# Optimization experiments

Hardware: AMD Instinct MI355X
Metric: run time of the kernel (lower is better)

The kernel has to match this reference:

```python
import jax, jax.numpy as jnp
import numpy as np

N_SAMPLES = 8388608  # total packed samples across all rays
N_RAYS = 131072      # number of rays (segments)


def setup_inputs() -> dict:
    key = jax.random.key(0)
    k1, k2, k3 = jax.random.split(key, 3)
    # Sorted segment ids emulate the packed ray layout (samples of a ray are contiguous).
    segment_ids = jnp.sort(
        jax.random.randint(k1, (N_SAMPLES,), 0, N_RAYS, dtype=jnp.int32)
    )
    rgb_samples = jax.random.normal(k2, (N_SAMPLES, 3), dtype=jnp.float32)
    weights_samples = jax.random.uniform(k3, (N_SAMPLES, 1), dtype=jnp.float32)
    return {
        "segment_ids": segment_ids,
        "rgb_samples": rgb_samples,
        "weights_samples": weights_samples,
        "n_rays": N_RAYS,
    }


def reference(segment_ids, rgb_samples, weights_samples, n_rays):
    # pred_rgb[r] = sum over samples s belonging to ray r of w_s * rgb_s
    weighted = rgb_samples * weights_samples  # [N,3], weight broadcast over channels
    pred_rgb = jax.ops.segment_sum(weighted, segment_ids, num_segments=n_rays)  # [n_rays,3]
    return pred_rgb
```

## Files before the change

kernel.cpp:

```cpp
#include <hip/hip_runtime.h>


#define NTHREADS 256
#define SPT 16

__global__ __launch_bounds__(NTHREADS) void zero_out_kernel(float4* __restrict__ out4,
                                                            int n4) {
  int i = blockIdx.x * blockDim.x + threadIdx.x;
  if (i < n4) out4[i] = make_float4(0.f, 0.f, 0.f, 0.f);
}

__global__ __launch_bounds__(NTHREADS) void integrate_kernel(
    const int* __restrict__ ids, const float* __restrict__ rgb,
    const float* __restrict__ w, float* __restrict__ out, int n_samples) {
  const int lane = threadIdx.x & 63;
  const long long base = (long long)(blockIdx.x * blockDim.x + threadIdx.x) * SPT;

  int idv[SPT];
  float px[SPT], py[SPT], pz[SPT];

  if (base + (SPT - 1) < (long long)n_samples) {
    float ww[SPT], rr[3 * SPT];
    #pragma unroll
    for (int b = 0; b < SPT / 4; ++b) {
      const int4 t = *(const int4*)(ids + base + 4 * b);
      idv[4 * b + 0] = t.x; idv[4 * b + 1] = t.y;
      idv[4 * b + 2] = t.z; idv[4 * b + 3] = t.w;
    }
    #pragma unroll
    for (int b = 0; b < SPT / 4; ++b) {
      const float4 t = *(const float4*)(w + base + 4 * b);
      ww[4 * b + 0] = t.x; ww[4 * b + 1] = t.y;
      ww[4 * b + 2] = t.z; ww[4 * b + 3] = t.w;
    }
    #pragma unroll
    for (int m = 0; m < 3 * SPT / 4; ++m) {
      const float4 t = *(const float4*)(rgb + 3 * base + 4 * m);
      rr[4 * m + 0] = t.x; rr[4 * m + 1] = t.y;
      rr[4 * m + 2] = t.z; rr[4 * m + 3] = t.w;
    }
    #pragma unroll
    for (int k = 0; k < SPT; ++k) {
      px[k] = rr[3 * k + 0] * ww[k];
      py[k] = rr[3 * k + 1] * ww[k];
      pz[k] = rr[3 * k + 2] * ww[k];
    }
  } else {
    const int last = ids[n_samples - 1];
    #pragma unroll
    for (int j = 0; j < SPT; ++j) {
      const long long s = base + j;
      if (s < n_samples) {
        idv[j] = ids[s];
        const float t = w[s];
        px[j] = rgb[3 * s + 0] * t;
        py[j] = rgb[3 * s + 1] * t;
        pz[j] = rgb[3 * s + 2] * t;
      } else {
        idv[j] = (j == 0) ? last : idv[j - 1];
        px[j] = py[j] = pz[j] = 0.f;
      }
    }
  }

  const int first_id = idv[0];
  int run_id = first_id;
  float rx = px[0], ry = py[0], rz = pz[0];
  float hx = 0.f, hy = 0.f, hz = 0.f;
  bool f_intra = false;
  #pragma unroll
  for (int k = 1; k < SPT; ++k) {
    if (idv[k] == run_id) {
      rx += px[k]; ry += py[k]; rz += pz[k];
    } else {
      if (!f_intra) {
        hx = rx; hy = ry; hz = rz; f_intra = true;
      } else {
        atomicAdd(&out[3 * run_id + 0], rx);
        atomicAdd(&out[3 * run_id + 1], ry);
        atomicAdd(&out[3 * run_id + 2], rz);
      }
      run_id = idv[k];
      rx = px[k]; ry = py[k]; rz = pz[k];
    }
  }
  const int last_id = run_id;

  const int prev_tid = __shfl_up(last_id, 1, 64);
  int fl = (lane == 0 || f_intra || prev_tid != first_id) ? 1 : 0;
  float sx = rx, sy = ry, sz = rz;
  #pragma unroll
  for (int off = 1; off < 64; off <<= 1) {
    const float ox = __shfl_up(sx, off, 64);
    const float oy = __shfl_up(sy, off, 64);
    const float oz = __shfl_up(sz, off, 64);
    const int ofl = __shfl_up(fl, off, 64);
    if (lane >= off && fl == 0) { sx += ox; sy += oy; sz += oz; fl = ofl; }
  }

  const float pSx = __shfl_up(sx, 1, 64);
  const float pSy = __shfl_up(sy, 1, 64);
  const float pSz = __shfl_up(sz, 1, 64);
  if (f_intra) {
    const bool link = (lane > 0) && (prev_tid == first_id);
    atomicAdd(&out[3 * first_id + 0], hx + (link ? pSx : 0.f));
    atomicAdd(&out[3 * first_id + 1], hy + (link ? pSy : 0.f));
    atomicAdd(&out[3 * first_id + 2], hz + (link ? pSz : 0.f));
  }

  const int next_hid = __shfl_down(first_id, 1, 64);
  if (lane == 63 || next_hid != last_id) {
    atomicAdd(&out[3 * last_id + 0], sx);
    atomicAdd(&out[3 * last_id + 1], sy);
    atomicAdd(&out[3 * last_id + 2], sz);
  }
}

extern "C" void kernel_launch(void* const* d_in, const int* in_sizes, int n_in,
                              void* d_out, int out_size, void* d_ws, size_t ws_size,
                              hipStream_t stream) {
  const int*   segment_ids = (const int*)d_in[0];
  const float* rgb         = (const float*)d_in[1];
  const float* weights     = (const float*)d_in[2];
  float*       out         = (float*)d_out;

  const int n_samples = in_sizes[0];

  {
    int n4 = out_size / 4;
    int blocks = (n4 + NTHREADS - 1) / NTHREADS;
    zero_out_kernel<<<blocks, NTHREADS, 0, stream>>>((float4*)out, n4);
  }
  {
    int spb = NTHREADS * SPT;
    int blocks = (n_samples + spb - 1) / spb;
    integrate_kernel<<<blocks, NTHREADS, 0, stream>>>(
        segment_ids, rgb, weights, out, n_samples);
  }
}
```

Baseline: 195.9 us.

## Restructure integration into per-wave coalesced chunks with double-buffered loads

Each wave now owns a span of eight 256-sample chunks with 4 samples per lane, so loads across lanes are contiguous instead of strided by 16 samples. Loads for the next chunk are issued before processing the current one, to overlap memory latency with the scan and atomics. The trade-off is a full wave shuffle scan per chunk and more boundary atomics between chunks.

Measured after the change: 201.8 us. 3.0% more time.

```diff
diff --git a/kernel.cpp b/kernel.cpp
--- a/kernel.cpp
+++ b/kernel.cpp
@@ -2,7 +2,11 @@
 
 
 #define NTHREADS 256
-#define SPT 16
+#define WAVES_PER_BLOCK (NTHREADS / 64)
+#define CPL 4
+#define CHUNK (64 * CPL)
+#define CHUNKS 8
+#define SPW (CHUNK * CHUNKS)
 
 __global__ __launch_bounds__(NTHREADS) void zero_out_kernel(float4* __restrict__ out4,
                                                             int n4) {
@@ -10,58 +14,16 @@
   if (i < n4) out4[i] = make_float4(0.f, 0.f, 0.f, 0.f);
 }
 
-__global__ __launch_bounds__(NTHREADS) void integrate_kernel(
-    const int* __restrict__ ids, const float* __restrict__ rgb,
-    const float* __restrict__ w, float* __restrict__ out, int n_samples) {
-  const int lane = threadIdx.x & 63;
-  const long long base = (long long)(blockIdx.x * blockDim.x + threadIdx.x) * SPT;
-
-  int idv[SPT];
-  float px[SPT], py[SPT], pz[SPT];
-
-  if (base + (SPT - 1) < (long long)n_samples) {
-    float ww[SPT], rr[3 * SPT];
-    #pragma unroll
-    for (int b = 0; b < SPT / 4; ++b) {
-      const int4 t = *(const int4*)(ids + base + 4 * b);
-      idv[4 * b + 0] = t.x; idv[4 * b + 1] = t.y;
-      idv[4 * b + 2] = t.z; idv[4 * b + 3] = t.w;
-    }
-    #pragma unroll
-    for (int b = 0; b < SPT / 4; ++b) {
-      const float4 t = *(const float4*)(w + base + 4 * b);
-      ww[4 * b + 0] = t.x; ww[4 * b + 1] = t.y;
-      ww[4 * b + 2] = t.z; ww[4 * b + 3] = t.w;
-    }
-    #pragma unroll
-    for (int m = 0; m < 3 * SPT / 4; ++m) {
-      const float4 t = *(const float4*)(rgb + 3 * base + 4 * m);
-      rr[4 * m + 0] = t.x; rr[4 * m + 1] = t.y;
-      rr[4 * m + 2] = t.z; rr[4 * m + 3] = t.w;
-    }
-    #pragma unroll
-    for (int k = 0; k < SPT; ++k) {
-      px[k] = rr[3 * k + 0] * ww[k];
-      py[k] = rr[3 * k + 1] * ww[k];
-      pz[k] = rr[3 * k + 2] * ww[k];
-    }
-  } else {
-    const int last = ids[n_samples - 1];
-    #pragma unroll
-    for (int j = 0; j < SPT; ++j) {
-      const long long s = base + j;
-      if (s < n_samples) {
-        idv[j] = ids[s];
-        const float t = w[s];
-        px[j] = rgb[3 * s + 0] * t;
-        py[j] = rgb[3 * s + 1] * t;
-        pz[j] = rgb[3 * s + 2] * t;
-      } else {
-        idv[j] = (j == 0) ? last : idv[j - 1];
-        px[j] = py[j] = pz[j] = 0.f;
-      }
-    }
-  }
+__device__ __forceinline__ void process_chunk(const int4 id4, const float4 w4,
+                                              const float4 r0, const float4 r1,
+                                              const float4 r2, const int lane,
+                                              float* __restrict__ out) {
+  int idv[CPL] = {id4.x, id4.y, id4.z, id4.w};
+  float px[CPL], py[CPL], pz[CPL];
+  px[0] = r0.x * w4.x; py[0] = r0.y * w4.x; pz[0] = r0.z * w4.x;
+  px[1] = r0.w * w4.y; py[1] = r1.x * w4.y; pz[1] = r1.y * w4.y;
+  px[2] = r1.z * w4.z; py[2] = r1.w * w4.z; pz[2] = r2.x * w4.z;
+  px[3] = r2.y * w4.w; py[3] = r2.z * w4.w; pz[3] = r2.w * w4.w;
 
   const int first_id = idv[0];
   int run_id = first_id;
@@ -69,7 +31,7 @@
   float hx = 0.f, hy = 0.f, hz = 0.f;
   bool f_intra = false;
   #pragma unroll
-  for (int k = 1; k < SPT; ++k) {
+  for (int k = 1; k < CPL; ++k) {
     if (idv[k] == run_id) {
       rx += px[k]; ry += py[k]; rz += pz[k];
     } else {
@@ -116,6 +78,68 @@
   }
 }
 
+__global__ __launch_bounds__(NTHREADS, 4) void integrate_kernel(
+    const int* __restrict__ ids, const float* __restrict__ rgb,
+    const float* __restrict__ w, float* __restrict__ out, int n_samples) {
+  const int lane = threadIdx.x & 63;
+  const long long wave_id =
+      (long long)blockIdx.x * WAVES_PER_BLOCK + (threadIdx.x >> 6);
+  const long long span0 = wave_id * SPW;
+  if (span0 >= (long long)n_samples) return;
+
+  if (span0 + SPW <= (long long)n_samples) {
+    const long long lb = span0 + (long long)lane * CPL;
+    int4 Ai; float4 Aw, Ar0, Ar1, Ar2;
+    int4 Bi; float4 Bw, Br0, Br1, Br2;
+#define LOADX(P, c)                                   \
+    do {                                              \
+      const long long b_ = lb + (long long)(c) * CHUNK; \
+      P##i  = *(const int4*)(ids + b_);               \
+      P##w  = *(const float4*)(w + b_);               \
+      P##r0 = *(const float4*)(rgb + 3 * b_);         \
+      P##r1 = *(const float4*)(rgb + 3 * b_ + 4);     \
+      P##r2 = *(const float4*)(rgb + 3 * b_ + 8);     \
+    } while (0)
+    LOADX(A, 0);
+    #pragma unroll
+    for (int c = 0; c < CHUNKS; c += 2) {
+      LOADX(B, c + 1);
+      process_chunk(Ai, Aw, Ar0, Ar1, Ar2, lane, out);
+      if (c + 2 < CHUNKS) LOADX(A, c + 2);
+      process_chunk(Bi, Bw, Br0, Br1, Br2, lane, out);
+    }
+#undef LOADX
+  } else {
+    const int last = ids[n_samples - 1];
+    for (int c = 0; c < CHUNKS; ++c) {
+      const long long cb = span0 + (long long)c * CHUNK;
+      if (cb >= (long long)n_samples) break;
+      int idt[CPL]; float wt[CPL], rt[3 * CPL];
+      #pragma unroll
+      for (int j = 0; j < CPL; ++j) {
+        const long long s = cb + (long long)lane * CPL + j;
+        if (s < (long long)n_samples) {
+          idt[j] = ids[s];
+          wt[j] = w[s];
+          rt[3 * j + 0] = rgb[3 * s + 0];
+          rt[3 * j + 1] = rgb[3 * s + 1];
+          rt[3 * j + 2] = rgb[3 * s + 2];
+        } else {
+          idt[j] = (j == 0) ? last : idt[j - 1];
+          wt[j] = 0.f;
+          rt[3 * j + 0] = rt[3 * j + 1] = rt[3 * j + 2] = 0.f;
+        }
+      }
+      const int4 i4 = make_int4(idt[0], idt[1], idt[2], idt[3]);
+      const float4 w4 = make_float4(wt[0], wt[1], wt[2], wt[3]);
+      const float4 r0 = make_float4(rt[0], rt[1], rt[2], rt[3]);
+      const float4 r1 = make_float4(rt[4], rt[5], rt[6], rt[7]);
+      const float4 r2 = make_float4(rt[8], rt[9], rt[10], rt[11]);
+      process_chunk(i4, w4, r0, r1, r2, lane, out);
+    }
+  }
+}
+
 extern "C" void kernel_launch(void* const* d_in, const int* in_sizes, int n_in,
                               void* d_out, int out_size, void* d_ws, size_t ws_size,
                               hipStream_t stream) {
@@ -132,8 +156,8 @@
     zero_out_kernel<<<blocks, NTHREADS, 0, stream>>>((float4*)out, n4);
   }
   {
-    int spb = NTHREADS * SPT;
-    int blocks = (n_samples + spb - 1) / spb;
+    long long waves = ((long long)n_samples + SPW - 1) / SPW;
+    int blocks = (int)((waves + WAVES_PER_BLOCK - 1) / WAVES_PER_BLOCK);
     integrate_kernel<<<blocks, NTHREADS, 0, stream>>>(
         segment_ids, rgb, weights, out, n_samples);
   }
```
